# Optimization experiments

Hardware: AMD Instinct MI355X
Metric: run time of the kernel (lower is better)

The kernel has to match this reference:

```python
import jax, jax.numpy as jnp
import numpy as np

B, N, D = 8, 8192, 512
H, WIDTH = 8, 2048
DH = D // H
EPS = 1e-5


def _ln(x, g, b):
    m = jnp.mean(x, axis=-1, keepdims=True)
    v = jnp.mean(jnp.square(x - m), axis=-1, keepdims=True)
    return (x - m) * jax.lax.rsqrt(v + EPS) * g + b


def setup_inputs() -> dict:
    key = jax.random.key(0)
    ks = jax.random.split(key, 16)
    s = 0.02
    return {
        "x": jax.random.normal(ks[0], (B, N, D), dtype=jnp.float32),
        "mask": jnp.ones((B, N), dtype=jnp.float32),
        "Wq": jax.random.normal(ks[1], (D, D), dtype=jnp.float32) * s,
        "bq": jnp.zeros((D,), dtype=jnp.float32),
        "Wk": jax.random.normal(ks[2], (D, D), dtype=jnp.float32) * s,
        "bk": jnp.zeros((D,), dtype=jnp.float32),
        "Wv": jax.random.normal(ks[3], (D, D), dtype=jnp.float32) * s,
        "bv": jnp.zeros((D,), dtype=jnp.float32),
        "q_alpha": jax.random.normal(ks[4], (H, DH), dtype=jnp.float32),
        "k_beta": jax.random.normal(ks[5], (H, DH), dtype=jnp.float32),
        "Wo": jax.random.normal(ks[6], (D, D), dtype=jnp.float32) * s,
        "bo": jnp.zeros((D,), dtype=jnp.float32),
        "ln0_g": jnp.ones((D,), dtype=jnp.float32),
        "ln0_b": jnp.zeros((D,), dtype=jnp.float32),
        "ln1_g": jnp.ones((D,), dtype=jnp.float32),
        "ln1_b": jnp.zeros((D,), dtype=jnp.float32),
        "W1": jax.random.normal(ks[7], (WIDTH, D), dtype=jnp.float32) * s,
        "b1": jnp.zeros((WIDTH,), dtype=jnp.float32),
        "W2": jax.random.normal(ks[8], (D, WIDTH), dtype=jnp.float32) * s,
        "b2": jnp.zeros((D,), dtype=jnp.float32),
    }


def reference(x, mask, Wq, bq, Wk, bk, Wv, bv, q_alpha, k_beta, Wo, bo,
              ln0_g, ln0_b, ln1_g, ln1_b, W1, b1, W2, b2):
    scale = DH ** -0.5
    mask_ = mask[..., None]                       # [B,N,1]
    valid = (mask != 0)[..., None]                # [B,N,1] bool, broadcast over H

    residual = x
    xn = _ln(x, ln0_g, ln0_b) * mask_

    Q = (xn @ Wq.T + bq).reshape(B, N, H, DH)
    K = (xn @ Wk.T + bk).reshape(B, N, H, DH)
    V = (xn @ Wv.T + bv).reshape(B, N, H, DH)

    # stage 1: global query pooling
    alpha = jnp.einsum('bnhd,hd->bnh', Q, q_alpha) * scale
    alpha = jnp.where(valid, alpha, -jnp.inf)
    alpha = jax.nn.softmax(alpha, axis=1)         # softmax over N
    global_q = jnp.einsum('bnhd,bnh->bhd', Q, alpha)

    # stage 2: global value pooling
    P = K * global_q[:, None]                     # [B,N,H,DH]
    beta = jnp.einsum('bnhd,hd->bnh', P, k_beta) * scale
    beta = jnp.where(valid, beta, -jnp.inf)
    beta = jax.nn.softmax(beta, axis=1)
    global_v = jnp.einsum('bnhd,bnh->bhd', V, beta)

    out = (Q + global_v[:, None]).reshape(B, N, D)
    out = out @ Wo.T + bo
    x = residual + out

    residual = x
    xn = _ln(x, ln1_g, ln1_b)
    h = jax.nn.gelu(xn @ W1.T + b1, approximate=False)
    h = jax.nn.gelu(h @ W2.T + b2, approximate=False)
    x = residual + h
    x = x * mask_
    return x
```

## Files before the change

### kernel.cpp

```cpp
#include <hip/hip_runtime.h>
#include <hip/hip_bf16.h>
#include <hip/hip_fp8.h>
#include <math.h>

typedef short s8v __attribute__((ext_vector_type(8)));
typedef short s4v __attribute__((ext_vector_type(4)));
typedef __bf16 bf8v __attribute__((ext_vector_type(8)));
typedef float f4v __attribute__((ext_vector_type(4)));
typedef long l2v __attribute__((ext_vector_type(2)));

#define GLOBAL_AS __attribute__((address_space(1)))
#define LDS_AS __attribute__((address_space(3)))

static __device__ __forceinline__ float bf2f(ushort u) {
  return __builtin_bit_cast(float, (unsigned int)u << 16);
}
static __device__ __forceinline__ ushort f2bf(float f) {
  unsigned int u = __builtin_bit_cast(unsigned int, f);
  u += 0x7FFFu + ((u >> 16) & 1u);
  return (ushort)(u >> 16);
}
static __device__ __forceinline__ unsigned char f2fp8(float f) {
#if __has_builtin(__builtin_amdgcn_cvt_pk_fp8_f32)
  int p = __builtin_amdgcn_cvt_pk_fp8_f32(f, f, 0, false);
  return (unsigned char)(p & 0xFF);
#else
  __hip_fp8_e4m3 v(f);
  return (unsigned char)v.__x;
#endif
}
static __device__ __forceinline__ float gelu_f(float v) {
  float t = v * v;
  float u = v * (0.0356774081f * t + 0.7978845608f);
  float e = __expf(-2.0f * u);
  return v * __builtin_amdgcn_rcpf(1.0f + e);
}
static __device__ __forceinline__ float wave_max_f(float v) {
  #pragma unroll
  for (int o = 32; o >= 1; o >>= 1) v = fmaxf(v, __shfl_xor(v, o));
  return v;
}
static __device__ __forceinline__ float wave_sum_f(float v) {
  #pragma unroll
  for (int o = 32; o >= 1; o >>= 1) v += __shfl_xor(v, o);
  return v;
}
static __device__ __forceinline__ void gload16(const void* g, const void* l) {
  __builtin_amdgcn_global_load_lds(
      (const GLOBAL_AS unsigned int*)g,
      (LDS_AS unsigned int*)l, 16, 0, 0);
}

__global__ void cvt_f32_fp8il(const float* __restrict__ in,
                              unsigned char* __restrict__ out, int n, int kmask) {
  int i = (blockIdx.x * 256 + threadIdx.x) * 4;
  if (i >= n) return;
  float4 v = *(const float4*)(in + i);
  const int k = i & kmask;
  const int r = k & 63;
  const int qq = (r >> 3) & 3, h = (r >> 5) & 1, j = r & 7;
  const long o = (long)(i - r) + qq * 16 + h * 8 + j;
  uchar4 ob;
  ob.x = f2fp8(v.x * 8.f); ob.y = f2fp8(v.y * 8.f);
  ob.z = f2fp8(v.z * 8.f); ob.w = f2fp8(v.w * 8.f);
  *(uchar4*)(out + o) = ob;
}

__global__ __launch_bounds__(256) void transpose512(
    const float* __restrict__ in, float* __restrict__ out) {
  __shared__ float t[32][33];
  const int bx = blockIdx.x & 15, by = blockIdx.x >> 4;
  const int tx = threadIdx.x & 31, ty = threadIdx.x >> 5;
  #pragma unroll
  for (int i = 0; i < 4; ++i)
    t[ty + i * 8][tx] = in[(long)(by * 32 + ty + i * 8) * 512 + bx * 32 + tx];
  __syncthreads();
  #pragma unroll
  for (int i = 0; i < 4; ++i)
    out[(long)(bx * 32 + ty + i * 8) * 512 + by * 32 + tx] = t[tx][ty + i * 8];
}

__global__ __launch_bounds__(256) void wqo_kernel(
    const float* __restrict__ Wo, const float* __restrict__ Wq,
    ushort* __restrict__ WqoB)
{
  __shared__ float lO[64][33];
  __shared__ float lQ[32][65];
  const int t = threadIdx.x;
  const int bi = (blockIdx.x & 7) * 64, bj = (blockIdx.x >> 3) * 64;
  float acc[16] = {};
  for (int k0 = 0; k0 < 512; k0 += 32) {
    __syncthreads();
    {
      const int r = t >> 2, c = (t & 3) * 8;
      #pragma unroll
      for (int j = 0; j < 8; ++j) lO[r][c + j] = Wo[(long)(bi + r) * 512 + k0 + c + j];
      const int r2 = t >> 3, c2 = (t & 7) * 8;
      #pragma unroll
      for (int j = 0; j < 8; ++j) lQ[r2][c2 + j] = Wq[(long)(k0 + r2) * 512 + bj + c2 + j];
    }
    __syncthreads();
    const int j = t & 63, ig = t >> 6;
    for (int kk = 0; kk < 32; ++kk) {
      float q = lQ[kk][j];
      #pragma unroll
      for (int ii = 0; ii < 16; ++ii) acc[ii] += lO[ig * 16 + ii][kk] * q;
    }
  }
  const int j = t & 63, ig = t >> 6;
  #pragma unroll
  for (int ii = 0; ii < 16; ++ii)
    WqoB[(long)(bi + ig * 16 + ii) * 512 + bj + j] = f2bf(acc[ii]);
}

__global__ __launch_bounds__(256) void wa_kernel(
    const float* __restrict__ qa, const float* __restrict__ Wq,
    const float* __restrict__ bqv, ushort* __restrict__ waB, float* __restrict__ ca)
{
  __shared__ float ql[64];
  const int h = blockIdx.x;
  const int t = threadIdx.x;
  if (h >= 8) {
    waB[h * 512 + t] = 0; waB[h * 512 + 256 + t] = 0;
    if (t == 0) ca[h] = 0.f;
    return;
  }
  if (t < 64) ql[t] = qa[h * 64 + t];
  __syncthreads();
  #pragma unroll
  for (int half = 0; half < 2; ++half) {
    const int k = half * 256 + t;
    float s = 0;
    for (int dd = 0; dd < 64; ++dd) s += ql[dd] * Wq[(long)(h * 64 + dd) * 512 + k];
    waB[h * 512 + k] = f2bf(s);
  }
  if (t == 0) {
    float s = 0;
    for (int dd = 0; dd < 64; ++dd) s += ql[dd] * bqv[h * 64 + dd];
    ca[h] = s;
  }
}

__global__ __launch_bounds__(256) void ln_rows(
    const float* __restrict__ x, const float* __restrict__ gam,
    const float* __restrict__ bet, const float* __restrict__ mask,
    ushort* __restrict__ out)
{
  const int tid = threadIdx.x, lane = tid & 63, wv = tid >> 6;
  const long row = (long)blockIdx.x * 4 + wv;
  const float* xp = x + row * 512 + lane * 8;
  float4 a = *(const float4*)xp;
  float4 b = *(const float4*)(xp + 4);
  float s = a.x + a.y + a.z + a.w + b.x + b.y + b.z + b.w;
  float q = a.x*a.x + a.y*a.y + a.z*a.z + a.w*a.w
          + b.x*b.x + b.y*b.y + b.z*b.z + b.w*b.w;
  s = wave_sum_f(s); q = wave_sum_f(q);
  float m = s * (1.f / 512.f);
  float var = q * (1.f / 512.f) - m * m;
  float r = rsqrtf(var + 1e-5f);
  float mk = mask ? mask[row] : 1.f;
  const float* gp = gam + lane * 8;
  const float* bp = bet + lane * 8;
  float4 g0 = *(const float4*)gp, g1 = *(const float4*)(gp + 4);
  float4 c0 = *(const float4*)bp, c1 = *(const float4*)(bp + 4);
  s8v o;
  o[0] = (short)f2bf(((a.x - m) * r * g0.x + c0.x) * mk);
  o[1] = (short)f2bf(((a.y - m) * r * g0.y + c0.y) * mk);
  o[2] = (short)f2bf(((a.z - m) * r * g0.z + c0.z) * mk);
  o[3] = (short)f2bf(((a.w - m) * r * g0.w + c0.w) * mk);
  o[4] = (short)f2bf(((b.x - m) * r * g1.x + c1.x) * mk);
  o[5] = (short)f2bf(((b.y - m) * r * g1.y + c1.y) * mk);
  o[6] = (short)f2bf(((b.z - m) * r * g1.z + c1.z) * mk);
  o[7] = (short)f2bf(((b.w - m) * r * g1.w + c1.w) * mk);
  *(s8v*)(out + row * 512 + lane * 8) = o;
}

__global__ __launch_bounds__(256) void ln_rows_fp8il(
    const ushort* __restrict__ x, const float* __restrict__ gam,
    const float* __restrict__ bet, unsigned char* __restrict__ out)
{
  const int tid = threadIdx.x, lane = tid & 63, wv = tid >> 6;
  const long row = (long)blockIdx.x * 4 + wv;
  s8v v = *(const s8v*)(x + row * 512 + lane * 8);
  float xv[8];
  #pragma unroll
  for (int j = 0; j < 8; ++j) xv[j] = bf2f((ushort)v[j]);
  float s = 0.f, q = 0.f;
  #pragma unroll
  for (int j = 0; j < 8; ++j) { s += xv[j]; q += xv[j] * xv[j]; }
  s = wave_sum_f(s); q = wave_sum_f(q);
  float m = s * (1.f / 512.f);
  float var = q * (1.f / 512.f) - m * m;
  float r = rsqrtf(var + 1e-5f);
  const float* gp = gam + lane * 8;
  const float* bp = bet + lane * 8;
  float4 g0 = *(const float4*)gp, g1 = *(const float4*)(gp + 4);
  float4 c0 = *(const float4*)bp, c1 = *(const float4*)(bp + 4);
  float gg[8] = {g0.x, g0.y, g0.z, g0.w, g1.x, g1.y, g1.z, g1.w};
  float cc[8] = {c0.x, c0.y, c0.z, c0.w, c1.x, c1.y, c1.z, c1.w};
  unsigned long long pk = 0;
  #pragma unroll
  for (int j = 0; j < 8; ++j) {
    unsigned char b8 = f2fp8((xv[j] - m) * r * gg[j] + cc[j]);
    pk |= (unsigned long long)b8 << (8 * j);
  }
  *(unsigned long long*)(out + row * 512 + (lane >> 3) * 64
                         + (lane & 3) * 16 + ((lane >> 2) & 1) * 8) = pk;
}

template<int BS, int CS>
__global__ __launch_bounds__(256) void logits_k(
    const ushort* __restrict__ XN, const ushort* __restrict__ Wl,
    const float* __restrict__ cvec, const float* __restrict__ mask,
    float* __restrict__ outL)
{
  __shared__ ushort lw[16 * 512];
  const int tid = threadIdx.x, lane = tid & 63, wv = tid >> 6;
  const long r0 = (long)blockIdx.x * 64;
  const int b = (int)(r0 >> 13);
  #pragma unroll
  for (int i = 0; i < 4; ++i) {
    const int u = tid + i * 256;
    const int h2 = u >> 6, uu = u & 63;
    s8v v = *(const s8v*)(Wl + (long)b * BS + h2 * 512 + uu * 8);
    *(s8v*)(lw + h2 * 512 + (uu ^ (h2 & 7)) * 8) = v;
  }
  __syncthreads();
  const int h = lane & 15, q = lane >> 4;
  const long rw = r0 + wv * 16;
  const ushort* ap = XN + (rw + (lane & 15)) * 512 + q * 8;
  f4v acc = {};
  #pragma unroll
  for (int t = 0; t < 16; ++t) {
    bf8v a = *(const bf8v*)(ap + t * 32);
    bf8v bb = *(const bf8v*)(lw + h * 512 + (((t * 4 + q) ^ (h & 7))) * 8);
    acc = __builtin_amdgcn_mfma_f32_16x16x32_bf16(a, bb, acc, 0, 0, 0);
  }
  const float cv = cvec[b * CS + h];
  #pragma unroll
  for (int j = 0; j < 4; ++j) {
    const long n = rw + q * 4 + j;
    float v = (acc[j] + cv) * 0.125f;
    if (mask[n] == 0.f) v = -1e30f;
    if (h < 8) outL[((long)((b << 3) + h) << 13) + (n & 8191)] = v;
  }
}

__global__ __launch_bounds__(1024) void softmax_rows(float* __restrict__ L)
{
  __shared__ float red[16];
  __shared__ float bc;
  const int tid = threadIdx.x, lane = tid & 63, wv = tid >> 6;
  float* p = L + ((long)blockIdx.x << 13) + tid * 8;
  float4 v0 = *(float4*)p;
  float4 v1 = *(float4*)(p + 4);
  float m = fmaxf(fmaxf(fmaxf(v0.x, v0.y), fmaxf(v0.z, v0.w)),
                  fmaxf(fmaxf(v1.x, v1.y), fmaxf(v1.z, v1.w)));
  m = wave_max_f(m);
  if (lane == 0) red[wv] = m;
  __syncthreads();
  if (tid < 64) {
    float t = (lane < 16) ? red[lane] : -INFINITY;
    t = wave_max_f(t);
    if (lane == 0) bc = t;
  }
  __syncthreads();
  const float gm = bc;
  v0.x = __expf(v0.x - gm); v0.y = __expf(v0.y - gm);
  v0.z = __expf(v0.z - gm); v0.w = __expf(v0.w - gm);
  v1.x = __expf(v1.x - gm); v1.y = __expf(v1.y - gm);
  v1.z = __expf(v1.z - gm); v1.w = __expf(v1.w - gm);
  float s = v0.x + v0.y + v0.z + v0.w + v1.x + v1.y + v1.z + v1.w;
  s = wave_sum_f(s);
  __syncthreads();
  if (lane == 0) red[wv] = s;
  __syncthreads();
  if (tid < 64) {
    float t = (lane < 16) ? red[lane] : 0.f;
    t = wave_sum_f(t);
    if (lane == 0) bc = t;
  }
  __syncthreads();
  const float inv = 1.0f / bc;
  v0.x *= inv; v0.y *= inv; v0.z *= inv; v0.w *= inv;
  v1.x *= inv; v1.y *= inv; v1.z *= inv; v1.w *= inv;
  *(float4*)p = v0;
  *(float4*)(p + 4) = v1;
}

__global__ __launch_bounds__(256) void pool_w(
    const ushort* __restrict__ XN, const float* __restrict__ wbuf,
    float* __restrict__ part)
{
  __shared__ float wlds[128][8];
  __shared__ float cmb[4][512];
  const int tid = threadIdx.x;
  const int b = blockIdx.x >> 6, ch = blockIdx.x & 63;
  const long g0 = ((long)b << 13) + ch * 128;
  if (tid < 128) {
    #pragma unroll
    for (int h = 0; h < 8; ++h)
      wlds[tid][h] = wbuf[(((long)(b * 8 + h)) << 13) + ch * 128 + tid];
  }
  __syncthreads();
  const int rg = tid >> 6, c8 = (tid & 63) * 8;
  f4v acc[8][2] = {};
  for (int it = 0; it < 32; ++it) {
    const int r = it * 4 + rg;
    s8v xv = *(const s8v*)(XN + (g0 + r) * 512 + c8);
    float xf[8];
    #pragma unroll
    for (int j = 0; j < 8; ++j) xf[j] = bf2f((ushort)xv[j]);
    #pragma unroll
    for (int h = 0; h < 8; ++h) {
      const float w = wlds[r][h];
      #pragma unroll
      for (int j = 0; j < 8; ++j) acc[h][j >> 2][j & 3] += w * xf[j];
    }
  }
  #pragma unroll
  for (int h = 0; h < 8; ++h) {
    __syncthreads();
    #pragma unroll
    for (int j = 0; j < 8; ++j) cmb[rg][c8 + j] = acc[h][j >> 2][j & 3];
    __syncthreads();
    const int col = tid * 2;
    float s0 = cmb[0][col] + cmb[1][col] + cmb[2][col] + cmb[3][col];
    float s1 = cmb[0][col + 1] + cmb[1][col + 1] + cmb[2][col + 1] + cmb[3][col + 1];
    *(float2*)(part + (((long)blockIdx.x * 8 + h) << 9) + col) = make_float2(s0, s1);
  }
}

__global__ __launch_bounds__(256) void combine_px(
    const float* __restrict__ part, float* __restrict__ px)
{
  const int bh = blockIdx.x;
  const int b = bh >> 3, h = bh & 7;
  const int col = threadIdx.x * 2;
  float s0 = 0.f, s1 = 0.f;
  for (int ch = 0; ch < 64; ++ch) {
    const float* p = part + (((long)((b * 64 + ch) * 8 + h)) << 9) + col;
    s0 += p[0]; s1 += p[1];
  }
  px[(bh << 9) + col] = s0;
  px[(bh << 9) + col + 1] = s1;
}

__global__ __launch_bounds__(64) void prep_gq_wb(
    const float* __restrict__ px, const float* __restrict__ WqT,
    const float* __restrict__ bqv, const float* __restrict__ kbv,
    const float* __restrict__ Wk, const float* __restrict__ bkv,
    ushort* __restrict__ wbB, float* __restrict__ cbs)
{
  __shared__ float pxl[512];
  __shared__ float gkb[64];
  const int bh = blockIdx.x, b = bh >> 3, h = bh & 7, d = threadIdx.x;
  #pragma unroll
  for (int i = 0; i < 8; ++i) pxl[d + i * 64] = px[(bh << 9) + d + i * 64];
  __syncthreads();
  float acc = bqv[h * 64 + d];
  for (int c = 0; c < 512; ++c) acc += pxl[c] * WqT[(long)c * 512 + h * 64 + d];
  gkb[d] = acc * kbv[h * 64 + d];
  __syncthreads();
  float s[8] = {};
  for (int dd = 0; dd < 64; ++dd) {
    const float g = gkb[dd];
    const float* wr = Wk + (long)(h * 64 + dd) * 512 + d;
    #pragma unroll
    for (int ki = 0; ki < 8; ++ki) s[ki] += g * wr[ki * 64];
  }
  #pragma unroll
  for (int ki = 0; ki < 8; ++ki)
    wbB[(long)(b * 16 + h) * 512 + d + ki * 64] = f2bf(s[ki]);
  if (d == 0) {
    float t = 0.f;
    for (int dd = 0; dd < 64; ++dd) t += gkb[dd] * bkv[h * 64 + dd];
    cbs[b * 16 + h] = t;
  }
  if (h == 0) {
    #pragma unroll
    for (int hp = 8; hp < 16; ++hp)
      for (int k = d; k < 512; k += 64) wbB[(long)(b * 16 + hp) * 512 + k] = 0;
    if (d < 8) cbs[b * 16 + 8 + d] = 0.f;
  }
}

__global__ __launch_bounds__(64) void prep_gv(
    const float* __restrict__ pv, const float* __restrict__ WvT,
    const float* __restrict__ bvv, const float* __restrict__ bqv,
    float* __restrict__ gvb)
{
  __shared__ float pxl[512];
  const int bh = blockIdx.x, b = bh >> 3, h = bh & 7, d = threadIdx.x;
  #pragma unroll
  for (int i = 0; i < 8; ++i) pxl[d + i * 64] = pv[(bh << 9) + d + i * 64];
  __syncthreads();
  float acc = bvv[h * 64 + d] + bqv[h * 64 + d];
  for (int c = 0; c < 512; ++c) acc += pxl[c] * WvT[(long)c * 512 + h * 64 + d];
  gvb[b * 512 + h * 64 + d] = acc;
}

__global__ __launch_bounds__(256) void bias_gv(
    const float* __restrict__ gv, const float* __restrict__ Wo,
    const float* __restrict__ bo, float* __restrict__ bo2) {
  const int b = blockIdx.x;
  const int n = blockIdx.y * 256 + threadIdx.x;
  const float* g = gv + b * 512;
  const float* w = Wo + (long)n * 512;
  float acc = 0.f;
  for (int d = 0; d < 512; d += 4) {
    float4 wv4 = *(const float4*)(w + d);
    acc += g[d] * wv4.x + g[d + 1] * wv4.y + g[d + 2] * wv4.z + g[d + 3] * wv4.w;
  }
  bo2[b * 512 + n] = bo[n] + acc;
}

#define MFMA_(d,a,b) d = __builtin_amdgcn_mfma_f32_16x16x32_bf16(a, b, d, 0, 0, 0)

template<int EPI, int LDA, int NN, int KK>
__global__ __launch_bounds__(512, 4) void gemmP(
    const ushort* __restrict__ A, const ushort* __restrict__ W,
    const float* __restrict__ bias, const void* __restrict__ resid,
    const float* __restrict__ mask, void* __restrict__ Out)
{
  constexpr int NBX = NN / 256;
  constexpr int NT = KK / 32;
  __shared__ __align__(16) ushort lds[3][12288];
  const int tid = threadIdx.x;
  const int lane = tid & 63;
  const int w = tid >> 6;
  const int wm = w >> 2, wn = w & 3;

  const int nwg = gridDim.x;
  const int cpx = nwg >> 3;
  const int wg = (blockIdx.x & 7) * cpx + (blockIdx.x >> 3);
  const int bx = wg % NBX, by = wg / NBX;
  const long bm = (long)by * 128;
  const int bn = bx * 256;

  const int scr = tid >> 2, sls = tid & 3;
  const int akU = ((sls ^ (scr & 3) ^ ((scr >> 2) & 3))) * 8;
  const ushort* asrc = A + (bm + scr) * (long)LDA + akU;
  const int rbe = (scr & 31) + ((scr >> 5) << 6);
  const ushort* besrc = W + (long)(bn + rbe) * KK + akU;
  const ushort* bosrc = W + (long)(bn + rbe + 32) * KK + akU;

#define STG(b_, Tt) { \
    gload16(asrc + (Tt) * 32, &lds[b_][tid * 8]); \
    gload16(besrc + (Tt) * 32, &lds[b_][4096 + tid * 8]); \
    gload16(bosrc + (Tt) * 32, &lds[b_][8192 + tid * 8]); }

  STG(0, 0);
  STG(1, 1);

  f4v acc[4][4] = {};

  const int L = lane & 15, q = lane >> 4;
  const int soff = (q ^ (lane & 3) ^ ((lane >> 2) & 3)) * 8;
  const int abase = (wm * 64 + L) * 32 + soff;
  const int bbase = 4096 + (wn * 32 + L) * 32 + soff;

  asm volatile("s_waitcnt vmcnt(3)" ::: "memory");
  asm volatile("s_barrier" ::: "memory");

  for (int T = 0; T < NT; ++T) {
    const ushort* Lp = &lds[T % 3][0];
    bf8v aR[4], bR[4];
    #pragma unroll
    for (int m = 0; m < 4; ++m) aR[m] = *(const bf8v*)(Lp + abase + m * 512);
    bR[0] = *(const bf8v*)(Lp + bbase);
    bR[1] = *(const bf8v*)(Lp + bbase + 512);
    bR[2] = *(const bf8v*)(Lp + bbase + 4096);
    bR[3] = *(const bf8v*)(Lp + bbase + 4096 + 512);
    if (T + 2 < NT) {
      STG((T + 2) % 3, T + 2);
      asm volatile("s_waitcnt vmcnt(3)" ::: "memory");
    } else {
      asm volatile("s_waitcnt vmcnt(0)" ::: "memory");
    }
    asm volatile("s_barrier" ::: "memory");
    __builtin_amdgcn_s_setprio(1);
    #pragma unroll
    for (int m = 0; m < 4; ++m)
      #pragma unroll
      for (int n = 0; n < 4; ++n)
        MFMA_(acc[m][n], aR[m], bR[n]);
    __builtin_amdgcn_s_setprio(0);
  }
#undef STG

  const int colb = bn + wn * 64 + L;
  const long rowb = bm + wm * 64 + q * 4;
  const float* biasp = bias + ((bm >> 13) << 9);
  #pragma unroll
  for (int m = 0; m < 4; ++m) {
    #pragma unroll
    for (int j = 0; j < 4; ++j) {
      const long row = rowb + m * 16 + j;
      #pragma unroll
      for (int n = 0; n < 4; ++n) {
        const int col = colb + n * 16;
        float v = acc[m][n][j] + biasp[col];
        const long idx = row * (long)NN + col;
        ((ushort*)Out)[idx] = f2bf(v + ((const float*)resid)[idx]);
      }
    }
  }
}

template<int EPI, int NN, int KK>
__global__ __launch_bounds__(512, 4) void gemmF8(
    const unsigned char* __restrict__ A, const unsigned char* __restrict__ W,
    const float* __restrict__ bias, const void* __restrict__ resid,
    const float* __restrict__ mask, void* __restrict__ Out)
{
  constexpr int NBX = NN / 256;
  constexpr int NT = KK / 64;
  __shared__ __align__(16) unsigned char lds8[2][24576];
  const int tid = threadIdx.x;
  const int lane = tid & 63;
  const int w = tid >> 6;
  const int wm = w >> 2, wn = w & 3;

  const int nwg = gridDim.x;
  const int cpx = nwg >> 3;
  const int wg = (blockIdx.x & 7) * cpx + (blockIdx.x >> 3);
  const int bx = wg % NBX, by = wg / NBX;
  const long bm = (long)by * 128;
  const int bn = bx * 256;

  const int srow = tid >> 2;
  const int sgu = (tid & 3) ^ ((srow >> 1) & 3);
  const unsigned char* asrc = A + (bm + srow) * (long)KK + sgu * 16;
  const unsigned char* b0src = W + (long)(bn + srow) * KK + sgu * 16;
  const unsigned char* b1src = W + (long)(bn + 128 + srow) * KK + sgu * 16;

#define STG8(bf_, Tt) { \
    gload16(asrc + (Tt) * 64, &lds8[bf_][tid * 16]); \
    gload16(b0src + (Tt) * 64, &lds8[bf_][8192 + tid * 16]); \
    gload16(b1src + (Tt) * 64, &lds8[bf_][16384 + tid * 16]); }

  STG8(0, 0);
  STG8(1, 1);

  f4v acc[4][4] = {};

  const int L = lane & 15, q = lane >> 4;
  const int ua = (q ^ ((L >> 1) & 3)) * 16;
  const int arow = (wm * 64 + L) * 64;
  const int brow = 8192 + (wn * 64 + L) * 64;

  asm volatile("s_waitcnt vmcnt(3)" ::: "memory");
  asm volatile("s_barrier" ::: "memory");

  for (int T = 0; T < NT; ++T) {
    const unsigned char* Lp = &lds8[T & 1][0];
    l2v aV[4], bV[4];
    #pragma unroll
    for (int m = 0; m < 4; ++m) aV[m] = *(const l2v*)(Lp + arow + m * 1024 + ua);
    #pragma unroll
    for (int n = 0; n < 4; ++n) bV[n] = *(const l2v*)(Lp + brow + n * 1024 + ua);
    asm volatile("s_barrier" ::: "memory");
    if (T + 2 < NT) {
      STG8(T & 1, T + 2);
      asm volatile("s_waitcnt vmcnt(3)" ::: "memory");
    } else {
      asm volatile("s_waitcnt vmcnt(0)" ::: "memory");
    }
    asm volatile("s_barrier" ::: "memory");
    __builtin_amdgcn_s_setprio(1);
    #pragma unroll
    for (int m = 0; m < 4; ++m)
      #pragma unroll
      for (int n = 0; n < 4; ++n) {
        acc[m][n] = __builtin_amdgcn_mfma_f32_16x16x32_fp8_fp8(
            aV[m][0], bV[n][0], acc[m][n], 0, 0, 0);
        acc[m][n] = __builtin_amdgcn_mfma_f32_16x16x32_fp8_fp8(
            aV[m][1], bV[n][1], acc[m][n], 0, 0, 0);
      }
    __builtin_amdgcn_s_setprio(0);
  }
#undef STG8

  const long rowb = bm + wm * 64 + q * 4;
  const int gbase = bn + wn * 64;
  #pragma unroll
  for (int m = 0; m < 4; ++m) {
    #pragma unroll
    for (int j = 0; j < 4; ++j) {
      const long row = rowb + m * 16 + j;
      float mk;
      if constexpr (EPI == 8) mk = mask[row];
      #pragma unroll
      for (int n = 0; n < 4; ++n) {
        const int col = gbase + n * 16 + L;
        float v = acc[m][n][j] * 0.125f + bias[col];
        if constexpr (EPI == 7) {
          const int rp = ((n * 2 + (L >> 3)) & 3) * 16 + (n >> 1) * 8 + (L & 7);
          ((unsigned char*)Out)[row * (long)NN + gbase + rp] = f2fp8(gelu_f(v));
        } else {
          const long idx = row * (long)NN + col;
          ((float*)Out)[idx] =
              (bf2f(((const ushort*)resid)[idx]) + gelu_f(v)) * mk;
        }
      }
    }
  }
}

extern "C" void kernel_launch(void* const* d_in, const int* in_sizes, int n_in,
                              void* d_out, int out_size, void* d_ws, size_t ws_size,
                              hipStream_t stream) {
  const float* x    = (const float*)d_in[0];
  const float* mask = (const float*)d_in[1];
  const float* Wq   = (const float*)d_in[2];
  const float* bq   = (const float*)d_in[3];
  const float* Wk   = (const float*)d_in[4];
  const float* bk   = (const float*)d_in[5];
  const float* Wv   = (const float*)d_in[6];
  const float* bv   = (const float*)d_in[7];
  const float* qa   = (const float*)d_in[8];
  const float* kb   = (const float*)d_in[9];
  const float* Wo   = (const float*)d_in[10];
  const float* bo   = (const float*)d_in[11];
  const float* g0   = (const float*)d_in[12];
  const float* be0  = (const float*)d_in[13];
  const float* g1   = (const float*)d_in[14];
  const float* be1  = (const float*)d_in[15];
  const float* W1   = (const float*)d_in[16];
  const float* b1   = (const float*)d_in[17];
  const float* W2   = (const float*)d_in[18];
  const float* b2   = (const float*)d_in[19];
  float* out = (float*)d_out;

  const int M = 65536;
  char* ws = (char*)d_ws;
  const size_t MB = 1024 * 1024;
  ushort* XN  = (ushort*)(ws);
  ushort* X1  = (ushort*)(ws + 64 * MB);
  unsigned char* XN1F = (unsigned char*)(ws + 128 * MB);
  unsigned char* H1F  = (unsigned char*)(ws + 192 * MB);
  float*  AL  = (float*)(ws + 320 * MB);
  float*  BL  = (float*)(ws + 322 * MB);
  float*  PART= (float*)(ws + 324 * MB);
  char* base = ws + 448 * MB;
  unsigned char* W1F = (unsigned char*)(base);
  unsigned char* W2F = (unsigned char*)(base + 2 * MB);
  ushort* WqoB = (ushort*)(base + 4 * MB);
  float*  WqT  = (float*)(base + 4 * MB + 512 * 1024);
  float*  WvT  = (float*)(base + 5 * MB + 512 * 1024);
  ushort* waB  = (ushort*)(base + 6 * MB + 512 * 1024);
  ushort* wbB  = (ushort*)(base + 6 * MB + 528 * 1024);
  float*  ca   = (float*)(base + 6 * MB + 656 * 1024);
  float*  cbs  = (float*)(base + 6 * MB + 660 * 1024);
  float*  PX   = (float*)(base + 6 * MB + 664 * 1024);
  float*  PV   = (float*)(base + 6 * MB + 792 * 1024);
  float*  GVB  = (float*)(base + 6 * MB + 920 * 1024);
  float*  BO2  = (float*)(base + 6 * MB + 936 * 1024);

  cvt_f32_fp8il<<<1024, 256, 0, stream>>>(W1, W1F, 1048576, 511);
  cvt_f32_fp8il<<<1024, 256, 0, stream>>>(W2, W2F, 1048576, 2047);
  wqo_kernel<<<64, 256, 0, stream>>>(Wo, Wq, WqoB);
  wa_kernel<<<16, 256, 0, stream>>>(qa, Wq, bq, waB, ca);
  transpose512<<<256, 256, 0, stream>>>(Wq, WqT);
  transpose512<<<256, 256, 0, stream>>>(Wv, WvT);

  ln_rows<<<M / 4, 256, 0, stream>>>(x, g0, be0, mask, XN);

  logits_k<0, 0><<<1024, 256, 0, stream>>>(XN, waB, ca, mask, AL);
  softmax_rows<<<64, 1024, 0, stream>>>(AL);
  pool_w<<<512, 256, 0, stream>>>(XN, AL, PART);
  combine_px<<<64, 256, 0, stream>>>(PART, PX);
  prep_gq_wb<<<64, 64, 0, stream>>>(PX, WqT, bq, kb, Wk, bk, wbB, cbs);

  logits_k<8192, 16><<<1024, 256, 0, stream>>>(XN, wbB, cbs, mask, BL);
  softmax_rows<<<64, 1024, 0, stream>>>(BL);
  pool_w<<<512, 256, 0, stream>>>(XN, BL, PART);
  combine_px<<<64, 256, 0, stream>>>(PART, PV);
  prep_gv<<<64, 64, 0, stream>>>(PV, WvT, bv, bq, GVB);
  bias_gv<<<dim3(8, 2), 256, 0, stream>>>(GVB, Wo, bo, BO2);

  gemmP<5, 512, 512, 512><<<2 * (M / 128), 512, 0, stream>>>(
      XN, WqoB, BO2, x, nullptr, X1);

  ln_rows_fp8il<<<M / 4, 256, 0, stream>>>(X1, g1, be1, XN1F);

  gemmF8<7, 2048, 512><<<8 * (M / 128), 512, 0, stream>>>(
      XN1F, W1F, b1, nullptr, nullptr, H1F);
  gemmF8<8, 512, 2048><<<2 * (M / 128), 512, 0, stream>>>(
      H1F, W2F, b2, X1, mask, out);
}
```

Baseline: 585.6 us.

## Permute W1 rows so FFN1 epilogue writes packed fp8 words; triple-buffer LDS

W1 is converted to fp8 with its output rows permuted, and b1 is permuted to match. Each lane of the first FFN GEMM then holds four contiguous interleaved output columns, so it can write one packed 32-bit fp8 word with paired cvt_pk instructions instead of four scattered byte stores. The gemmF8 LDS staging grows from two to three buffers, which removes one barrier per k-step. This raises LDS use to 72KB per block and may reduce occupancy, and it adds two small preprocessing launches.

```diff
diff --git a/kernel.cpp b/kernel.cpp
--- a/kernel.cpp
+++ b/kernel.cpp
@@ -64,6 +64,30 @@
   ob.x = f2fp8(v.x * 8.f); ob.y = f2fp8(v.y * 8.f);
   ob.z = f2fp8(v.z * 8.f); ob.w = f2fp8(v.w * 8.f);
   *(uchar4*)(out + o) = ob;
+}
+
+__global__ void cvt_w1_fp8il(const float* __restrict__ in,
+                             unsigned char* __restrict__ out) {
+  int i = (blockIdx.x * 256 + threadIdx.x) * 4;
+  const int ro = i >> 9;
+  const int k4 = i & 511;
+  const int g = ro >> 6, fr = ro & 63;
+  const int L = fr & 15, nn = fr >> 4;
+  const int sr = g * 64 + ((L >> 1) & 1) * 32 + (L >> 2) * 8 + (L & 1) * 4 + nn;
+  float4 v = *(const float4*)(in + (long)sr * 512 + k4);
+  const int r = k4 & 63;
+  const int o = (k4 - r) + ((r >> 3) & 3) * 16 + (r >> 5) * 8 + (r & 7);
+  uchar4 ob;
+  ob.x = f2fp8(v.x * 8.f); ob.y = f2fp8(v.y * 8.f);
+  ob.z = f2fp8(v.z * 8.f); ob.w = f2fp8(v.w * 8.f);
+  *(uchar4*)(out + (long)ro * 512 + o) = ob;
+}
+
+__global__ void perm_b1(const float* __restrict__ b1, float* __restrict__ b1p) {
+  const int p = blockIdx.x * 256 + threadIdx.x;
+  const int g = p >> 6, r = p & 63;
+  const int kc = ((r >> 3) & 1) * 32 + (r >> 4) * 8 + ((r >> 2) & 1) * 4 + (r & 3);
+  b1p[p] = b1[g * 64 + kc];
 }
 
 __global__ __launch_bounds__(256) void transpose512(
@@ -516,7 +540,7 @@
 {
   constexpr int NBX = NN / 256;
   constexpr int NT = KK / 64;
-  __shared__ __align__(16) unsigned char lds8[2][24576];
+  __shared__ __align__(16) unsigned char lds8[3][24576];
   const int tid = threadIdx.x;
   const int lane = tid & 63;
   const int w = tid >> 6;
@@ -554,15 +578,14 @@
   asm volatile("s_barrier" ::: "memory");
 
   for (int T = 0; T < NT; ++T) {
-    const unsigned char* Lp = &lds8[T & 1][0];
+    const unsigned char* Lp = &lds8[T % 3][0];
     l2v aV[4], bV[4];
     #pragma unroll
     for (int m = 0; m < 4; ++m) aV[m] = *(const l2v*)(Lp + arow + m * 1024 + ua);
     #pragma unroll
     for (int n = 0; n < 4; ++n) bV[n] = *(const l2v*)(Lp + brow + n * 1024 + ua);
-    asm volatile("s_barrier" ::: "memory");
     if (T + 2 < NT) {
-      STG8(T & 1, T + 2);
+      STG8((T + 2) % 3, T + 2);
       asm volatile("s_waitcnt vmcnt(3)" ::: "memory");
     } else {
       asm volatile("s_waitcnt vmcnt(0)" ::: "memory");
@@ -584,21 +607,39 @@
 
   const long rowb = bm + wm * 64 + q * 4;
   const int gbase = bn + wn * 64;
-  #pragma unroll
-  for (int m = 0; m < 4; ++m) {
-    #pragma unroll
-    for (int j = 0; j < 4; ++j) {
-      const long row = rowb + m * 16 + j;
-      float mk;
-      if constexpr (EPI == 8) mk = mask[row];
-      #pragma unroll
-      for (int n = 0; n < 4; ++n) {
-        const int col = gbase + n * 16 + L;
-        float v = acc[m][n][j] * 0.125f + bias[col];
-        if constexpr (EPI == 7) {
-          const int rp = ((n * 2 + (L >> 3)) & 3) * 16 + (n >> 1) * 8 + (L & 7);
-          ((unsigned char*)Out)[row * (long)NN + gbase + rp] = f2fp8(gelu_f(v));
-        } else {
+  if constexpr (EPI == 7) {
+    const float4 bp4 = *(const float4*)(bias + gbase + 4 * L);
+    #pragma unroll
+    for (int m = 0; m < 4; ++m) {
+      #pragma unroll
+      for (int j = 0; j < 4; ++j) {
+        const long row = rowb + m * 16 + j;
+        float e0 = gelu_f(acc[m][0][j] * 0.125f + bp4.x);
+        float e1 = gelu_f(acc[m][1][j] * 0.125f + bp4.y);
+        float e2 = gelu_f(acc[m][2][j] * 0.125f + bp4.z);
+        float e3 = gelu_f(acc[m][3][j] * 0.125f + bp4.w);
+        unsigned int pw;
+#if __has_builtin(__builtin_amdgcn_cvt_pk_fp8_f32)
+        int t0 = __builtin_amdgcn_cvt_pk_fp8_f32(e0, e1, 0, false);
+        pw = (unsigned int)__builtin_amdgcn_cvt_pk_fp8_f32(e2, e3, t0, true);
+#else
+        pw = (unsigned int)f2fp8(e0) | ((unsigned int)f2fp8(e1) << 8)
+           | ((unsigned int)f2fp8(e2) << 16) | ((unsigned int)f2fp8(e3) << 24);
+#endif
+        *(unsigned int*)((unsigned char*)Out + row * (long)NN + gbase + 4 * L) = pw;
+      }
+    }
+  } else {
+    #pragma unroll
+    for (int m = 0; m < 4; ++m) {
+      #pragma unroll
+      for (int j = 0; j < 4; ++j) {
+        const long row = rowb + m * 16 + j;
+        const float mk = mask[row];
+        #pragma unroll
+        for (int n = 0; n < 4; ++n) {
+          const int col = gbase + n * 16 + L;
+          float v = acc[m][n][j] * 0.125f + bias[col];
           const long idx = row * (long)NN + col;
           ((float*)Out)[idx] =
               (bf2f(((const ushort*)resid)[idx]) + gelu_f(v)) * mk;
@@ -657,8 +698,10 @@
   float*  PV   = (float*)(base + 6 * MB + 792 * 1024);
   float*  GVB  = (float*)(base + 6 * MB + 920 * 1024);
   float*  BO2  = (float*)(base + 6 * MB + 936 * 1024);
-
-  cvt_f32_fp8il<<<1024, 256, 0, stream>>>(W1, W1F, 1048576, 511);
+  float*  B1P  = (float*)(base + 6 * MB + 952 * 1024);
+
+  cvt_w1_fp8il<<<1024, 256, 0, stream>>>(W1, W1F);
+  perm_b1<<<8, 256, 0, stream>>>(b1, B1P);
   cvt_f32_fp8il<<<1024, 256, 0, stream>>>(W2, W2F, 1048576, 2047);
   wqo_kernel<<<64, 256, 0, stream>>>(Wo, Wq, WqoB);
   wa_kernel<<<16, 256, 0, stream>>>(qa, Wq, bq, waB, ca);
@@ -686,7 +729,7 @@
   ln_rows_fp8il<<<M / 4, 256, 0, stream>>>(X1, g1, be1, XN1F);
 
   gemmF8<7, 2048, 512><<<8 * (M / 128), 512, 0, stream>>>(
-      XN1F, W1F, b1, nullptr, nullptr, H1F);
+      XN1F, W1F, B1P, nullptr, nullptr, H1F);
   gemmF8<8, 512, 2048><<<2 * (M / 128), 512, 0, stream>>>(
       H1F, W2F, b2, X1, mask, out);
 }
```

Measured after the change: 590.4 us. Within noise of the previous version (+0.8%).
